# Kernel tuning notes

Hardware: AMD Instinct MI355X
Metric: run time of the kernel (lower is better)

The kernel has to match this reference:

```python
import jax, jax.numpy as jnp
import numpy as np

B, S, C = 1, 6, 128
Hf, Wf = 56, 100            # feature map (stride-8 of 448x800)
IMG_H, IMG_W = 448, 800
Z, Y, X = 128, 8, 128
BOUNDS = (-50.0, 50.0, -5.0, 5.0, -50.0, 50.0)
CENTROID = (0.0, 0.1, 0.0)
EPS = 1e-6


def _voxel_centers():
    # ref-frame (cam0) coordinates of voxel centers, Vox_util.Mem2Ref of gridcloud3d
    xmin, xmax = BOUNDS[0] + CENTROID[0], BOUNDS[1] + CENTROID[0]
    ymin, ymax = BOUNDS[2] + CENTROID[1], BOUNDS[3] + CENTROID[1]
    zmin, zmax = BOUNDS[4] + CENTROID[2], BOUNDS[5] + CENTROID[2]
    vsx, vsy, vsz = (xmax - xmin) / X, (ymax - ymin) / Y, (zmax - zmin) / Z
    zi, yi, xi = jnp.meshgrid(jnp.arange(Z), jnp.arange(Y), jnp.arange(X), indexing='ij')
    xr = xmin + vsx * 0.5 + xi.astype(jnp.float32) * vsx
    yr = ymin + vsy * 0.5 + yi.astype(jnp.float32) * vsy
    zr = zmin + vsz * 0.5 + zi.astype(jnp.float32) * vsz
    return jnp.stack([xr.reshape(-1), yr.reshape(-1), zr.reshape(-1)], axis=-1)  # (N,3), N=Z*Y*X


def setup_inputs() -> dict:
    key = jax.random.key(0)
    k1, k2 = jax.random.split(key)
    cam_feat = jax.random.normal(k1, (B, S, C, Hf, Wf), dtype=jnp.float32)
    # intrinsics: fx=fy=500, principal point at image center
    K = np.zeros((B, S, 4, 4), np.float32)
    K[..., 0, 0] = 500.0; K[..., 1, 1] = 500.0
    K[..., 0, 2] = IMG_W / 2.0; K[..., 1, 2] = IMG_H / 2.0
    K[..., 2, 2] = 1.0; K[..., 3, 3] = 1.0
    # surround-view rig: rotate about y (camera-frame vertical) by 2*pi*s/S
    ang = np.arange(S) * (2.0 * np.pi / S)
    c, s = np.cos(ang).astype(np.float32), np.sin(ang).astype(np.float32)
    R = np.zeros((B, S, 3, 3), np.float32)
    R[..., 0, 0] = c; R[..., 0, 2] = s; R[..., 1, 1] = 1.0
    R[..., 2, 0] = -s; R[..., 2, 2] = c
    t = np.stack([0.5 * s, np.full(S, -1.0, np.float32), 0.5 * c], axis=-1)[None].astype(np.float32)
    conv_w = jax.random.normal(k2, (C, C * Y, 3, 3), dtype=jnp.float32) * 0.02
    return {
        'cam_feat': cam_feat,
        'intrins': jnp.asarray(K),
        'rots': jnp.asarray(R),
        'trans': jnp.asarray(t),
        'conv_w': conv_w,
    }


def reference(cam_feat, intrins, rots, trans, conv_w):
    Bn, Sn = cam_feat.shape[:2]
    BS = Bn * Sn
    # velo_T_cams = [R|t]; cam0_T_camXs = inv(velo_T_cams[:,0]) @ velo_T_cams
    velo_T = (jnp.zeros((Bn, Sn, 4, 4), cam_feat.dtype)
              .at[..., :3, :3].set(rots)
              .at[..., :3, 3].set(trans)
              .at[..., 3, 3].set(1.0))
    cam0_T_camXs = jnp.einsum('bij,bsjk->bsik', jnp.linalg.inv(velo_T[:, 0]), velo_T)
    camXs_T_cam0 = jnp.linalg.inv(cam0_T_camXs)  # (B,S,4,4)
    # scale_intrinsics to feature resolution
    sx, sy = Wf / float(IMG_W), Hf / float(IMG_H)
    Kf = (jnp.zeros((Bn, Sn, 4, 4), cam_feat.dtype)
          .at[..., 0, 0].set(intrins[..., 0, 0] * sx)
          .at[..., 1, 1].set(intrins[..., 1, 1] * sy)
          .at[..., 0, 2].set(intrins[..., 0, 2] * sx)
          .at[..., 1, 2].set(intrins[..., 1, 2] * sy)
          .at[..., 2, 2].set(1.0).at[..., 3, 3].set(1.0))
    pixB_T_cam0 = jnp.einsum('bsij,bsjk->bsik', Kf, camXs_T_cam0).reshape(BS, 4, 4)
    camXs_T_cam0 = camXs_T_cam0.reshape(BS, 4, 4)

    xyz = _voxel_centers()                                   # (N,3)
    xyz1 = jnp.concatenate([xyz, jnp.ones((xyz.shape[0], 1), xyz.dtype)], axis=-1)  # (N,4)
    cam_pts = jnp.einsum('pij,nj->pni', camXs_T_cam0, xyz1)  # (BS,N,4)
    z = cam_pts[..., 2]
    pix = jnp.einsum('pij,nj->pni', pixB_T_cam0, xyz1)       # (BS,N,4)
    denom = jnp.maximum(pix[..., 2:3], EPS)
    x = pix[..., 0] / denom[..., 0]
    y = pix[..., 1] / denom[..., 0]
    valid = (x > -0.5) & (x < Wf - 0.5) & (y > -0.5) & (y < Hf - 0.5) & (z > 0.0)

    # normalize_grid2d + grid_sample(align_corners=False) unnormalization
    gx = jnp.clip(2.0 * x / (Wf - 1) - 1.0, -2.0, 2.0)
    gy = jnp.clip(2.0 * y / (Hf - 1) - 1.0, -2.0, 2.0)
    ux = ((gx + 1.0) * Wf - 1.0) * 0.5
    uy = ((gy + 1.0) * Hf - 1.0) * 0.5
    x0f, y0f = jnp.floor(ux), jnp.floor(uy)
    wx, wy = ux - x0f, uy - y0f
    x0i, y0i = x0f.astype(jnp.int32), y0f.astype(jnp.int32)

    feat = cam_feat.reshape(BS, C, Hf * Wf)

    def corner(xi, yi, w):
        inb = (xi >= 0) & (xi < Wf) & (yi >= 0) & (yi < Hf)  # zeros padding
        idx = jnp.clip(yi, 0, Hf - 1) * Wf + jnp.clip(xi, 0, Wf - 1)
        v = jnp.take_along_axis(feat, idx[:, None, :], axis=2)  # (BS,C,N)
        return v * (w * inb.astype(w.dtype))[:, None, :]

    vals = (corner(x0i, y0i, (1 - wx) * (1 - wy))
            + corner(x0i + 1, y0i, wx * (1 - wy))
            + corner(x0i, y0i + 1, (1 - wx) * wy)
            + corner(x0i + 1, y0i + 1, wx * wy))
    vals = vals * valid[:, None, :].astype(vals.dtype)
    feat_mems = vals.reshape(Bn, Sn, C, Z, Y, X)

    # reduce_masked_mean over cameras
    mask = (jnp.abs(feat_mems) > 0).astype(feat_mems.dtype)
    feat_mem = jnp.sum(feat_mems * mask, axis=1) / (EPS + jnp.sum(mask, axis=1))  # (B,C,Z,Y,X)

    # BEV compress: permute(0,1,3,2,4) -> (B, C*Y, Z, X), conv3x3 + InstanceNorm + GELU
    bev = jnp.transpose(feat_mem, (0, 1, 3, 2, 4)).reshape(Bn, C * Y, Z, X)
    out = jax.lax.conv_general_dilated(bev, conv_w, (1, 1), 'SAME',
                                       dimension_numbers=('NCHW', 'OIHW', 'NCHW'))
    mu = out.mean(axis=(2, 3), keepdims=True)
    var = out.var(axis=(2, 3), keepdims=True)
    out = (out - mu) * jax.lax.rsqrt(var + 1e-5)
    return jax.nn.gelu(out, approximate=False)
```

## Files before the change

### kernel.cpp

```cpp
#include <hip/hip_runtime.h>
#include <cmath>

#define SNUM 6
#define CNUM 128
#define HF 56
#define WF 100
#define HW (HF*WF)
#define ZN 128
#define YN 8
#define XN 128
#define NVOX (ZN*YN*XN)

typedef __attribute__((ext_vector_type(8))) short bf16x8;
typedef __attribute__((ext_vector_type(4))) float f32x4;
typedef __attribute__((ext_vector_type(4))) int   i32x4;

__device__ __forceinline__ unsigned short f2bf(float f) {
    unsigned u = __builtin_bit_cast(unsigned, f);
    unsigned r = (u + 0x7FFFu + ((u >> 16) & 1u)) >> 16;
    return (unsigned short)r;
}
__device__ __forceinline__ float bf2f(unsigned short h) {
    unsigned u = (unsigned)h << 16;
    return __builtin_bit_cast(float, u);
}

__device__ __forceinline__ void gl_lds16(const void* g, void* l) {
    __builtin_amdgcn_global_load_lds(
        (const __attribute__((address_space(1))) void*)g,
        (__attribute__((address_space(3))) void*)l, 16, 0, 0);
}
__device__ __forceinline__ void gl_lds4(const void* g, void* l) {
    __builtin_amdgcn_global_load_lds(
        (const __attribute__((address_space(1))) void*)g,
        (__attribute__((address_space(3))) void*)l, 4, 0, 0);
}

__global__ void k_setup(const float* __restrict__ intrins,
                        const float* __restrict__ rots,
                        const float* __restrict__ trans,
                        float* __restrict__ mats) {
    int s = threadIdx.x;
    if (s >= SNUM) return;
    float R0[9], Rs[9], t0[3], ts[3];
    for (int i = 0; i < 9; ++i) { R0[i] = rots[i]; Rs[i] = rots[s*9 + i]; }
    for (int i = 0; i < 3; ++i) { t0[i] = trans[i]; ts[i] = trans[s*3 + i]; }
    float M[3][4];
    float d0 = t0[0]-ts[0], d1 = t0[1]-ts[1], d2 = t0[2]-ts[2];
    for (int i = 0; i < 3; ++i) {
        for (int j = 0; j < 3; ++j)
            M[i][j] = Rs[0*3+i]*R0[0*3+j] + Rs[1*3+i]*R0[1*3+j] + Rs[2*3+i]*R0[2*3+j];
        M[i][3] = Rs[0*3+i]*d0 + Rs[1*3+i]*d1 + Rs[2*3+i]*d2;
    }
    const float sx = (float)WF/800.0f, sy = (float)HF/448.0f;
    float fx = intrins[s*16 + 0]*sx, fy = intrins[s*16 + 5]*sy;
    float cx = intrins[s*16 + 2]*sx, cy = intrins[s*16 + 6]*sy;
    float* o = mats + s*24;
    for (int j = 0; j < 4; ++j) {
        o[0*4+j]      = M[0][j];
        o[1*4+j]      = M[1][j];
        o[2*4+j]      = M[2][j];
        o[12 + 0*4+j] = fx*M[0][j] + cx*M[2][j];
        o[12 + 1*4+j] = fy*M[1][j] + cy*M[2][j];
        o[12 + 2*4+j] = M[2][j];
    }
}

__global__ __launch_bounds__(256) void k_tfeat(const float* __restrict__ cf,
                                               unsigned short* __restrict__ featT) {
    __shared__ float t[32][33];
    int s = blockIdx.z;
    int p0 = blockIdx.x * 32, c0 = blockIdx.y * 32;
    int tx = threadIdx.x, ty = threadIdx.y;
#pragma unroll
    for (int k = 0; k < 4; ++k) {
        int r = ty + k*8;
        t[r][tx] = cf[((size_t)s*CNUM + c0 + r)*HW + p0 + tx];
    }
    __syncthreads();
#pragma unroll
    for (int k = 0; k < 4; ++k) {
        int r = ty + k*8;
        featT[((size_t)s*HW + p0 + r)*CNUM + c0 + tx] = f2bf(t[tx][r]);
    }
}

__global__ __launch_bounds__(256) void k_zero(unsigned short* __restrict__ bevin2) {
    int i = blockIdx.x*256 + threadIdx.x;
    if (i >= 66048) return;
    size_t unit;
    if (i < 33280) {
        int zr = i / 16640;
        int j  = i - zr*16640;
        unit = (size_t)(zr ? 129 : 0)*16640 + j;
    } else {
        int j  = i - 33280;
        int zp = 1 + (j >> 8);
        int r  = j & 255;
        int c  = r >> 1;
        int xp = (r & 1) ? 129 : 0;
        unit = ((size_t)zp*128 + c)*130 + xp;
    }
    *(i32x4*)&bevin2[unit*8] = i32x4{0,0,0,0};
}

__global__ __launch_bounds__(256) void k_sample(const unsigned short* __restrict__ featT,
                                                const float* __restrict__ mats,
                                                unsigned short* __restrict__ bevin2) {
#pragma clang fp contract(off)
    __shared__ float xch[16][132];
    __shared__ float2 suv[16][6];
    const int tid = threadIdx.x;
    const int b = blockIdx.x;
    const int z = b >> 6, x0 = (b & 63) * 2;
    const int cl = tid & 15, vs = tid >> 4;
    if (tid < 96) {
        int v = tid / 6, s = tid - (tid/6)*6;
        int yi = v >> 1, xi2 = x0 + (v & 1);
        float xr = -49.609375f + (float)xi2 * 0.78125f;
        float yr = (-4.9f + 0.625f) + (float)yi * 1.25f;
        float zr = -49.609375f + (float)z * 0.78125f;
        const float* m = mats + s*24;
        float zc = m[8]*xr  + m[9]*yr  + m[10]*zr + m[11];
        float ph = m[12]*xr + m[13]*yr + m[14]*zr + m[15];
        float qh = m[16]*xr + m[17]*yr + m[18]*zr + m[19];
        float denom = fmaxf(zc, 1e-6f);
        float px = ph / denom, py = qh / denom;
        bool valid = (px > -0.5f) & (px < (float)WF - 0.5f) &
                     (py > -0.5f) & (py < (float)HF - 0.5f) & (zc > 0.0f);
        float ux = -10000.0f, uy = -10000.0f;
        if (valid) {
            float gx = 2.0f*px/((float)WF - 1.0f) - 1.0f;
            float gy = 2.0f*py/((float)HF - 1.0f) - 1.0f;
            gx = fminf(fmaxf(gx, -2.0f), 2.0f);
            gy = fminf(fmaxf(gy, -2.0f), 2.0f);
            ux = ((gx + 1.0f)*(float)WF - 1.0f)*0.5f;
            uy = ((gy + 1.0f)*(float)HF - 1.0f)*0.5f;
        }
        suv[v][s] = float2{ux, uy};
    }
    __syncthreads();

    const bf16x8 zz8 = {0,0,0,0,0,0,0,0};
    float sum[8], cnt[8];
#pragma unroll
    for (int k = 0; k < 8; ++k) { sum[k] = 0.0f; cnt[k] = 0.0f; }
    for (int s = 0; s < SNUM; ++s) {
        float2 u = suv[vs][s];
        if (u.x < -999.0f) continue;
        float x0f = floorf(u.x), y0f = floorf(u.y);
        float wx = u.x - x0f, wy = u.y - y0f;
        int ix = (int)x0f, iy = (int)y0f;
        float w00 = (1.0f-wx)*(1.0f-wy), w10 = wx*(1.0f-wy);
        float w01 = (1.0f-wx)*wy,        w11 = wx*wy;
        bool bx0 = (ix >= 0) & (ix < WF);
        bool bx1 = (ix >= -1) & (ix < WF-1);
        bool by0 = (iy >= 0) & (iy < HF);
        bool by1 = (iy >= -1) & (iy < HF-1);
        bool c00 = bx0 & by0, c10 = bx1 & by0, c01 = bx0 & by1, c11 = bx1 & by1;
        const unsigned short* fb = featT + (size_t)s * (HW*CNUM) + cl*8;
        long r0 = (long)(iy*WF + ix) * CNUM;
        bf16x8 v00 = c00 ? *(const bf16x8*)(fb + r0)                 : zz8;
        bf16x8 v10 = c10 ? *(const bf16x8*)(fb + r0 + CNUM)          : zz8;
        bf16x8 v01 = c01 ? *(const bf16x8*)(fb + r0 + WF*CNUM)       : zz8;
        bf16x8 v11 = c11 ? *(const bf16x8*)(fb + r0 + WF*CNUM + CNUM): zz8;
#pragma unroll
        for (int k = 0; k < 8; ++k) {
            float v = 0.0f;
            v = v + w00 * bf2f((unsigned short)v00[k]);
            v = v + w10 * bf2f((unsigned short)v10[k]);
            v = v + w01 * bf2f((unsigned short)v01[k]);
            v = v + w11 * bf2f((unsigned short)v11[k]);
            sum[k] += v;
            cnt[k] += (v != 0.0f) ? 1.0f : 0.0f;
        }
    }
#pragma unroll
    for (int k = 0; k < 8; ++k)
        xch[vs][cl*8 + k] = sum[k] / (1e-6f + cnt[k]);
    __syncthreads();
    {
        int c = tid >> 1, xs2 = tid & 1;
        unsigned pk[4];
#pragma unroll
        for (int j = 0; j < 4; ++j) {
            float v0 = xch[(2*j)*2 + xs2][c];
            float v1 = xch[(2*j+1)*2 + xs2][c];
            pk[j] = (unsigned)f2bf(v0) | ((unsigned)f2bf(v1) << 16);
        }
        size_t unit = ((size_t)(z+1)*128 + c)*130 + (x0 + xs2 + 1);
        *(i32x4*)&bevin2[unit*8] = i32x4{(int)pk[0], (int)pk[1], (int)pk[2], (int)pk[3]};
    }
}

__global__ __launch_bounds__(256) void k_wprep(const float* __restrict__ w,
                                               unsigned short* __restrict__ w2) {
    int i = blockIdx.x*256 + threadIdx.x;
    if (i >= 9*128*1024) return;
    int ci = i & 1023; int rest = i >> 10; int co = rest & 127; int tap = rest >> 7;
    w2[i] = f2bf(w[((size_t)co*1024 + ci)*9 + tap]);
}

__global__ __launch_bounds__(256, 1) void k_conv_mfma(
        const unsigned short* __restrict__ bevin2,
        const unsigned short* __restrict__ w2,
        float* __restrict__ out,
        float* __restrict__ psum, float* __restrict__ psq) {
    __shared__ __align__(16) unsigned short lds[4][12*144*8];
    const int tid  = threadIdx.x;
    const int bid  = blockIdx.x;
    const int swz  = (bid & 7)*32 + (bid >> 3);
    const int z0   = swz & 127;
    const int coh  = swz >> 7;
    const int lane = tid & 63, wid = tid >> 6;
    const int wr = wid >> 1, xw = wid & 1;
    const int co_base = coh*64 + wr*32;
    const int l15 = lane & 15, lhi = lane >> 4;

    f32x4 acc[2][4];
#pragma unroll
    for (int f = 0; f < 2; ++f)
#pragma unroll
        for (int nf = 0; nf < 4; ++nf) acc[f][nf] = f32x4{0.f,0.f,0.f,0.f};

    const unsigned short* aw0 = w2 + ((size_t)(co_base      + l15))*1024 + lhi*8;
    const unsigned short* aw1 = w2 + ((size_t)(co_base + 16 + l15))*1024 + lhi*8;

    bf16x8 aC[6], aN[6];

#define STAGE(STEP)                                                            \
    {                                                                          \
        _Pragma("unroll")                                                      \
        for (int r3 = 0; r3 < 3; ++r3) {                                       \
            int r = wid*3 + r3;                                                \
            int zrel = r >> 2, cq = r & 3;                                     \
            const unsigned short* gsrc = bevin2 +                              \
                (((size_t)(z0 + zrel)*128 + (STEP)*4 + cq)*130)*8;             \
            unsigned short* ldst = &lds[(STEP) & 3][r*144*8];                  \
            gl_lds16(gsrc + (size_t)lane*8, ldst);                             \
            gl_lds16(gsrc + (size_t)(64 + lane)*8, ldst + 64*8);               \
            gl_lds4 (gsrc + 128*8 + (size_t)lane*2, ldst + 128*8);             \
        }                                                                      \
    }
#define A6(DST, DZ, CI0)                                                       \
    {                                                                          \
        _Pragma("unroll")                                                      \
        for (int t = 0; t < 3; ++t) {                                          \
            DST[t*2+0] = *(const bf16x8*)(aw0 + (size_t)((DZ)*3+t)*131072 + (CI0)); \
            DST[t*2+1] = *(const bf16x8*)(aw1 + (size_t)((DZ)*3+t)*131072 + (CI0)); \
        }                                                                      \
    }
#define CDZ(DZ, BUF, AFR)                                                      \
    {                                                                          \
        _Pragma("unroll")                                                      \
        for (int dx = 0; dx < 3; ++dx) {                                       \
            bf16x8 a0 = AFR[dx*2+0];                                           \
            bf16x8 a1 = AFR[dx*2+1];                                           \
            _Pragma("unroll")                                                  \
            for (int nf = 0; nf < 4; ++nf) {                                   \
                bf16x8 bfr = *(const bf16x8*)&lds[BUF][(((DZ)*4 + lhi)*144 + xw*64 + nf*16 + l15 + dx)*8]; \
                acc[0][nf] = __builtin_amdgcn_mfma_f32_16x16x32_bf16(a0, bfr, acc[0][nf], 0, 0, 0); \
                acc[1][nf] = __builtin_amdgcn_mfma_f32_16x16x32_bf16(a1, bfr, acc[1][nf], 0, 0, 0); \
            }                                                                  \
        }                                                                      \
    }
#define PIPE_WAIT()  asm volatile("s_waitcnt vmcnt(24)" ::: "memory")

    STAGE(0); STAGE(1); STAGE(2);
    A6(aC, 0, 0);

    for (int p = 0; p < 16; ++p) {
        const int s = 2*p;
        PIPE_WAIT();
        __builtin_amdgcn_s_barrier();
        if (s + 3 < 32) STAGE(s + 3);
        A6(aN, 1, s*32);          CDZ(0, (s & 3), aC);
        A6(aC, 2, s*32);          CDZ(1, (s & 3), aN);
        A6(aN, 0, (s+1)*32);      CDZ(2, (s & 3), aC);
        PIPE_WAIT();
        __builtin_amdgcn_s_barrier();
        if (s + 4 < 32) STAGE(s + 4);
        A6(aC, 1, (s+1)*32);      CDZ(0, ((s+1) & 3), aN);
        A6(aN, 2, (s+1)*32);      CDZ(1, ((s+1) & 3), aC);
        if (s + 2 < 32) A6(aC, 0, (s+2)*32);
        CDZ(2, ((s+1) & 3), aN);
    }

    float ps[2][4], pq[2][4];
#pragma unroll
    for (int f = 0; f < 2; ++f)
#pragma unroll
        for (int r = 0; r < 4; ++r) { ps[f][r] = 0.0f; pq[f][r] = 0.0f; }
#pragma unroll
    for (int f = 0; f < 2; ++f)
#pragma unroll
        for (int nf = 0; nf < 4; ++nf)
#pragma unroll
            for (int r = 0; r < 4; ++r) {
                int co = co_base + f*16 + lhi*4 + r;
                float v = acc[f][nf][r];
                out[(size_t)co*16384 + z0*128 + xw*64 + nf*16 + l15] = v;
                ps[f][r] += v;
                pq[f][r] += v*v;
            }
#pragma unroll
    for (int f = 0; f < 2; ++f)
#pragma unroll
        for (int r = 0; r < 4; ++r) {
            float s = ps[f][r], q = pq[f][r];
#pragma unroll
            for (int m = 1; m < 16; m <<= 1) {
                s += __shfl_xor(s, m);
                q += __shfl_xor(q, m);
            }
            if (l15 == 0) {
                int co = co_base + f*16 + lhi*4 + r;
                int pb = z0*2 + xw;
                psum[co*256 + pb] = s;
                psq [co*256 + pb] = q;
            }
        }
#undef STAGE
#undef A6
#undef CDZ
#undef PIPE_WAIT
}

__global__ __launch_bounds__(256) void k_stats(const float* __restrict__ psum,
                                               const float* __restrict__ psq,
                                               float* __restrict__ stats) {
    __shared__ float r1[256], r2[256];
    int co = blockIdx.x, tid = threadIdx.x;
    r1[tid] = psum[co*256 + tid];
    r2[tid] = psq [co*256 + tid];
    __syncthreads();
    for (int off = 128; off > 0; off >>= 1) {
        if (tid < off) { r1[tid] += r1[tid+off]; r2[tid] += r2[tid+off]; }
        __syncthreads();
    }
    if (tid == 0) {
        float mean = r1[0] * (1.0f/16384.0f);
        float var  = r2[0] * (1.0f/16384.0f) - mean*mean;
        stats[co*2]   = mean;
        stats[co*2+1] = rsqrtf(var + 1e-5f);
    }
}

__global__ __launch_bounds__(256) void k_gelu(float* __restrict__ out,
                                              const float* __restrict__ stats) {
    int i = blockIdx.x*256 + threadIdx.x;
    int co = i >> 14;
    float v = out[i];
    float r = (v - stats[co*2]) * stats[co*2+1];
    out[i] = 0.5f * r * (1.0f + erff(r * 0.70710678118654752f));
}

extern "C" void kernel_launch(void* const* d_in, const int* in_sizes, int n_in,
                              void* d_out, int out_size, void* d_ws, size_t ws_size,
                              hipStream_t stream) {
    const float* cam_feat = (const float*)d_in[0];
    const float* intrins  = (const float*)d_in[1];
    const float* rots     = (const float*)d_in[2];
    const float* trans    = (const float*)d_in[3];
    const float* conv_w   = (const float*)d_in[4];
    float* out = (float*)d_out;
    float* ws  = (float*)d_ws;

    float* mats  = ws;
    unsigned short* featT  = (unsigned short*)(ws + 160);
    unsigned short* bevin2 = featT + (size_t)SNUM*HW*CNUM;
    unsigned short* w2     = bevin2 + (size_t)130*128*130*8;
    float* psum  = (float*)(w2 + 9*128*1024);
    float* psq   = psum + 32768;
    float* stats = psq + 32768;

    hipLaunchKernelGGL(k_setup, dim3(1), dim3(64), 0, stream, intrins, rots, trans, mats);
    hipLaunchKernelGGL(k_tfeat, dim3(HW/32, CNUM/32, SNUM), dim3(32,8), 0, stream, cam_feat, featT);
    hipLaunchKernelGGL(k_wprep, dim3((9*128*1024 + 255)/256), dim3(256), 0, stream, conv_w, w2);
    hipLaunchKernelGGL(k_zero, dim3((66048 + 255)/256), dim3(256), 0, stream, bevin2);
    hipLaunchKernelGGL(k_sample, dim3(8192), dim3(256), 0, stream, featT, mats, bevin2);
    hipLaunchKernelGGL(k_conv_mfma, dim3(256), dim3(256), 0, stream, bevin2, w2, out, psum, psq);
    hipLaunchKernelGGL(k_stats, dim3(128), dim3(256), 0, stream, psum, psq, stats);
    hipLaunchKernelGGL(k_gelu, dim3(8192), dim3(256), 0, stream, out, stats);
}
```

Baseline: 155.8 us.

## Use 8 waves per conv block with staggered LDS staging and MFMA priority

The MFMA conv kernel now runs 512 threads (8 waves) per block, each wave covering half as many x columns, so per-wave accumulators shrink and more waves are available to hide latency. The LDS staging of future input slices is spread across three wave phases between MFMA sections, with barriers around each section and s_setprio raising priority during MFMA bursts. The prefetch depth drops from three stages to two and the partial-stat buffers double to match the new wave count. Each wave now loads the same weight fragments for half the MFMA work, doubling weight global traffic per MFMA, and the added barriers could stall waves.

Result: slower. 207.6 us (+33.3%).

```diff
diff --git a/kernel.cpp b/kernel.cpp
--- a/kernel.cpp
+++ b/kernel.cpp
@@ -201,7 +201,7 @@
     w2[i] = f2bf(w[((size_t)co*1024 + ci)*9 + tap]);
 }
 
-__global__ __launch_bounds__(256, 1) void k_conv_mfma(
+__global__ __launch_bounds__(512, 2) void k_conv_mfma(
         const unsigned short* __restrict__ bevin2,
         const unsigned short* __restrict__ w2,
         float* __restrict__ out,
@@ -213,33 +213,37 @@
     const int z0   = swz & 127;
     const int coh  = swz >> 7;
     const int lane = tid & 63, wid = tid >> 6;
-    const int wr = wid >> 1, xw = wid & 1;
+    const int wr = wid >> 2, xw = wid & 3;
     const int co_base = coh*64 + wr*32;
     const int l15 = lane & 15, lhi = lane >> 4;
-
-    f32x4 acc[2][4];
+    const int sphase = wid % 3;
+
+    f32x4 acc[2][2];
 #pragma unroll
     for (int f = 0; f < 2; ++f)
 #pragma unroll
-        for (int nf = 0; nf < 4; ++nf) acc[f][nf] = f32x4{0.f,0.f,0.f,0.f};
+        for (int nf = 0; nf < 2; ++nf) acc[f][nf] = f32x4{0.f,0.f,0.f,0.f};
 
     const unsigned short* aw0 = w2 + ((size_t)(co_base      + l15))*1024 + lhi*8;
     const unsigned short* aw1 = w2 + ((size_t)(co_base + 16 + l15))*1024 + lhi*8;
 
     bf16x8 aC[6], aN[6];
 
-#define STAGE(STEP)                                                            \
+#define STG(SS)                                                                \
     {                                                                          \
         _Pragma("unroll")                                                      \
-        for (int r3 = 0; r3 < 3; ++r3) {                                       \
-            int r = wid*3 + r3;                                                \
-            int zrel = r >> 2, cq = r & 3;                                     \
-            const unsigned short* gsrc = bevin2 +                              \
-                (((size_t)(z0 + zrel)*128 + (STEP)*4 + cq)*130)*8;             \
-            unsigned short* ldst = &lds[(STEP) & 3][r*144*8];                  \
-            gl_lds16(gsrc + (size_t)lane*8, ldst);                             \
-            gl_lds16(gsrc + (size_t)(64 + lane)*8, ldst + 64*8);               \
-            gl_lds4 (gsrc + 128*8 + (size_t)lane*2, ldst + 128*8);             \
+        for (int k = 0; k < 5; ++k) {                                          \
+            int j = wid + 8*k;                                                 \
+            if (j < 36) {                                                      \
+                int r = j/3, part = j - r*3;                                   \
+                int zrel = r >> 2, cq = r & 3;                                 \
+                const unsigned short* gsrc = bevin2 +                          \
+                    (((size_t)(z0 + zrel)*128 + (SS)*4 + cq)*130)*8;           \
+                unsigned short* ldst = &lds[(SS) & 3][r*144*8];                \
+                if (part == 0)      gl_lds16(gsrc + (size_t)lane*8, ldst);     \
+                else if (part == 1) gl_lds16(gsrc + (size_t)(64 + lane)*8, ldst + 64*8); \
+                else                gl_lds4 (gsrc + 128*8 + (size_t)lane*2, ldst + 128*8); \
+            }                                                                  \
         }                                                                      \
     }
 #define A6(DST, DZ, CI0)                                                       \
@@ -250,40 +254,51 @@
             DST[t*2+1] = *(const bf16x8*)(aw1 + (size_t)((DZ)*3+t)*131072 + (CI0)); \
         }                                                                      \
     }
-#define CDZ(DZ, BUF, AFR)                                                      \
+#define MM(DZ, BUF, AFR)                                                       \
     {                                                                          \
+        __builtin_amdgcn_s_setprio(1);                                         \
         _Pragma("unroll")                                                      \
         for (int dx = 0; dx < 3; ++dx) {                                       \
             bf16x8 a0 = AFR[dx*2+0];                                           \
             bf16x8 a1 = AFR[dx*2+1];                                           \
             _Pragma("unroll")                                                  \
-            for (int nf = 0; nf < 4; ++nf) {                                   \
-                bf16x8 bfr = *(const bf16x8*)&lds[BUF][(((DZ)*4 + lhi)*144 + xw*64 + nf*16 + l15 + dx)*8]; \
+            for (int nf = 0; nf < 2; ++nf) {                                   \
+                bf16x8 bfr = *(const bf16x8*)&lds[BUF][(((DZ)*4 + lhi)*144 + xw*32 + nf*16 + l15 + dx)*8]; \
                 acc[0][nf] = __builtin_amdgcn_mfma_f32_16x16x32_bf16(a0, bfr, acc[0][nf], 0, 0, 0); \
                 acc[1][nf] = __builtin_amdgcn_mfma_f32_16x16x32_bf16(a1, bfr, acc[1][nf], 0, 0, 0); \
             }                                                                  \
         }                                                                      \
-    }
-#define PIPE_WAIT()  asm volatile("s_waitcnt vmcnt(24)" ::: "memory")
-
-    STAGE(0); STAGE(1); STAGE(2);
+        __builtin_amdgcn_s_setprio(0);                                         \
+    }
+#define BAR() __builtin_amdgcn_s_barrier()
+#define PIPE_WAIT()  asm volatile("s_waitcnt vmcnt(11)" ::: "memory")
+
+    STG(0); STG(1);
     A6(aC, 0, 0);
-
-    for (int p = 0; p < 16; ++p) {
-        const int s = 2*p;
+    __syncthreads();
+
+    for (int p2 = 0; p2 < 16; ++p2) {
+        const int s = 2*p2;
         PIPE_WAIT();
-        __builtin_amdgcn_s_barrier();
-        if (s + 3 < 32) STAGE(s + 3);
-        A6(aN, 1, s*32);          CDZ(0, (s & 3), aC);
-        A6(aC, 2, s*32);          CDZ(1, (s & 3), aN);
-        A6(aN, 0, (s+1)*32);      CDZ(2, (s & 3), aC);
+        A6(aN, 1, s*32);
+        if (sphase == 0 && s + 2 < 32) STG(s + 2);
+        BAR(); MM(0, (s & 3), aC); BAR();
+        A6(aC, 2, s*32);
+        if (sphase == 1 && s + 2 < 32) STG(s + 2);
+        BAR(); MM(1, (s & 3), aN); BAR();
+        A6(aN, 0, (s+1)*32);
+        if (sphase == 2 && s + 2 < 32) STG(s + 2);
+        BAR(); MM(2, (s & 3), aC); BAR();
         PIPE_WAIT();
-        __builtin_amdgcn_s_barrier();
-        if (s + 4 < 32) STAGE(s + 4);
-        A6(aC, 1, (s+1)*32);      CDZ(0, ((s+1) & 3), aN);
-        A6(aN, 2, (s+1)*32);      CDZ(1, ((s+1) & 3), aC);
+        A6(aC, 1, (s+1)*32);
+        if (sphase == 0 && s + 3 < 32) STG(s + 3);
+        BAR(); MM(0, ((s+1) & 3), aN); BAR();
+        A6(aN, 2, (s+1)*32);
+        if (sphase == 1 && s + 3 < 32) STG(s + 3);
+        BAR(); MM(1, ((s+1) & 3), aC); BAR();
         if (s + 2 < 32) A6(aC, 0, (s+2)*32);
-        CDZ(2, ((s+1) & 3), aN);
+        if (sphase == 2 && s + 3 < 32) STG(s + 3);
+        BAR(); MM(2, ((s+1) & 3), aN); BAR();
     }
 
     float ps[2][4], pq[2][4];
@@ -294,12 +309,12 @@
 #pragma unroll
     for (int f = 0; f < 2; ++f)
 #pragma unroll
-        for (int nf = 0; nf < 4; ++nf)
+        for (int nf = 0; nf < 2; ++nf)
 #pragma unroll
             for (int r = 0; r < 4; ++r) {
                 int co = co_base + f*16 + lhi*4 + r;
                 float v = acc[f][nf][r];
-                out[(size_t)co*16384 + z0*128 + xw*64 + nf*16 + l15] = v;
+                out[(size_t)co*16384 + z0*128 + xw*32 + nf*16 + l15] = v;
                 ps[f][r] += v;
                 pq[f][r] += v*v;
             }
@@ -315,14 +330,15 @@
             }
             if (l15 == 0) {
                 int co = co_base + f*16 + lhi*4 + r;
-                int pb = z0*2 + xw;
-                psum[co*256 + pb] = s;
-                psq [co*256 + pb] = q;
+                int pb = z0*4 + xw;
+                psum[co*512 + pb] = s;
+                psq [co*512 + pb] = q;
             }
         }
-#undef STAGE
+#undef STG
 #undef A6
-#undef CDZ
+#undef MM
+#undef BAR
 #undef PIPE_WAIT
 }
 
@@ -331,8 +347,8 @@
                                                float* __restrict__ stats) {
     __shared__ float r1[256], r2[256];
     int co = blockIdx.x, tid = threadIdx.x;
-    r1[tid] = psum[co*256 + tid];
-    r2[tid] = psq [co*256 + tid];
+    r1[tid] = psum[co*512 + tid] + psum[co*512 + 256 + tid];
+    r2[tid] = psq [co*512 + tid] + psq [co*512 + 256 + tid];
     __syncthreads();
     for (int off = 128; off > 0; off >>= 1) {
         if (tid < off) { r1[tid] += r1[tid+off]; r2[tid] += r2[tid+off]; }
@@ -371,15 +387,15 @@
     unsigned short* bevin2 = featT + (size_t)SNUM*HW*CNUM;
     unsigned short* w2     = bevin2 + (size_t)130*128*130*8;
     float* psum  = (float*)(w2 + 9*128*1024);
-    float* psq   = psum + 32768;
-    float* stats = psq + 32768;
+    float* psq   = psum + 65536;
+    float* stats = psq + 65536;
 
     hipLaunchKernelGGL(k_setup, dim3(1), dim3(64), 0, stream, intrins, rots, trans, mats);
     hipLaunchKernelGGL(k_tfeat, dim3(HW/32, CNUM/32, SNUM), dim3(32,8), 0, stream, cam_feat, featT);
     hipLaunchKernelGGL(k_wprep, dim3((9*128*1024 + 255)/256), dim3(256), 0, stream, conv_w, w2);
     hipLaunchKernelGGL(k_zero, dim3((66048 + 255)/256), dim3(256), 0, stream, bevin2);
     hipLaunchKernelGGL(k_sample, dim3(8192), dim3(256), 0, stream, featT, mats, bevin2);
-    hipLaunchKernelGGL(k_conv_mfma, dim3(256), dim3(256), 0, stream, bevin2, w2, out, psum, psq);
+    hipLaunchKernelGGL(k_conv_mfma, dim3(256), dim3(512), 0, stream, bevin2, w2, out, psum, psq);
     hipLaunchKernelGGL(k_stats, dim3(128), dim3(256), 0, stream, psum, psq, stats);
     hipLaunchKernelGGL(k_gelu, dim3(8192), dim3(256), 0, stream, out, stats);
 }
```
